# Kernel tuning notes

Measured on AMD Instinct MI355X. Metric: run time of the kernel, lower is better.

The kernel has to match this reference:

```python
import jax, jax.numpy as jnp
import numpy as np

WINDOW = (7, 7)
SHIFT = (3, 3)
NUM_HEADS = 4
DIM = 128


def _rel_pos_index():
    wh, ww = WINDOW
    coords = np.stack(np.meshgrid(np.arange(wh), np.arange(ww), indexing='ij'))  # [2,wh,ww]
    cf = coords.reshape(2, -1)                    # [2, N]
    rc = (cf[:, :, None] - cf[:, None, :]).transpose(1, 2, 0)  # [N,N,2]
    rc[:, :, 0] += wh - 1
    rc[:, :, 1] += ww - 1
    rc[:, :, 0] *= 2 * ww - 1
    return jnp.asarray(rc.sum(-1).reshape(-1))    # [N*N] int


def _attn_mask_np(pH, pW, sh):
    # Static-shape shift mask (host-side numpy; constant under jit).
    wh, ww = WINDOW
    m = np.zeros((pH, pW))
    h_slices = ((0, pH - wh), (pH - wh, pH - sh[0]), (pH - sh[0], pH))
    w_slices = ((0, pW - ww), (pW - ww, pW - sh[1]), (pW - sh[1], pW))
    cnt = 0
    for hs in h_slices:
        for ws in w_slices:
            m[hs[0]:hs[1], ws[0]:ws[1]] = cnt
            cnt += 1
    m = m.reshape(pH // wh, wh, pW // ww, ww).transpose(0, 2, 1, 3).reshape(-1, wh * ww)
    diff = m[:, None, :] - m[:, :, None]          # [num_windows, N, N]
    return jnp.asarray(np.where(diff != 0, -100.0, 0.0), dtype=np.float32)


def setup_inputs() -> dict:
    key = jax.random.key(0)
    ks = jax.random.split(key, 9)
    B, H, W, C = 32, 56, 56, DIM
    return {
        'input_q': jax.random.normal(ks[0], (B, H, W, C), jnp.float32),
        'input_k': jax.random.normal(ks[1], (B, H, W, C), jnp.float32),
        'input_v': jax.random.normal(ks[2], (B, H, W, C), jnp.float32),
        'q_weight': jax.random.normal(ks[3], (C, C), jnp.float32) * 0.05,
        'q_bias': jnp.zeros((C,), jnp.float32),
        'k_weight': jax.random.normal(ks[4], (C, C), jnp.float32) * 0.05,
        'k_bias': jnp.zeros((C,), jnp.float32),
        'v_weight': jax.random.normal(ks[5], (C, C), jnp.float32) * 0.05,
        'v_bias': jnp.zeros((C,), jnp.float32),
        'proj_weight': jax.random.normal(ks[6], (C, C), jnp.float32) * 0.05,
        'proj_bias': jnp.zeros((C,), jnp.float32),
        'rpb_table': jax.random.normal(ks[7], ((2 * WINDOW[0] - 1) * (2 * WINDOW[1] - 1), NUM_HEADS), jnp.float32) * 0.02,
    }


def reference(input_q, input_k, input_v, q_weight, q_bias, k_weight, k_bias,
              v_weight, v_bias, proj_weight, proj_bias, rpb_table):
    B, H, W, C = input_q.shape
    wh, ww = WINDOW
    pad_b = (wh - H % wh) % wh
    pad_r = (ww - W % ww) % ww
    pad = lambda t: jnp.pad(t, ((0, 0), (0, pad_b), (0, pad_r), (0, 0)))
    qx, kx, vx = pad(input_q), pad(input_k), pad(input_v)
    pad_H, pad_W = H + pad_b, W + pad_r
    sh = [0 if wh >= pad_H else SHIFT[0], 0 if ww >= pad_W else SHIFT[1]]
    if sum(sh) > 0:
        roll = lambda t: jnp.roll(t, (-sh[0], -sh[1]), axis=(1, 2))
        qx, kx, vx = roll(qx), roll(kx), roll(vx)
    nWh, nWw = pad_H // wh, pad_W // ww
    num_windows = nWh * nWw
    N = wh * ww

    def part(t):  # [B,pH,pW,C] -> [B*num_windows, N, C]
        t = t.reshape(B, nWh, wh, nWw, ww, C).transpose(0, 1, 3, 2, 4, 5)
        return t.reshape(B * num_windows, N, C)

    qx, kx, vx = part(qx), part(kx), part(vx)
    hd = C // NUM_HEADS

    def heads(x, w, b):  # linear + split heads -> [BW, nH, N, hd]
        return (x @ w.T + b).reshape(-1, N, NUM_HEADS, hd).transpose(0, 2, 1, 3)

    q = heads(qx, q_weight, q_bias) * (hd ** -0.5)
    k = heads(kx, k_weight, k_bias)
    v = heads(vx, v_weight, v_bias)

    attn = jnp.einsum('whqd,whkd->whqk', q, k)    # [BW, nH, N, N]
    rpb = rpb_table[_rel_pos_index()].reshape(N, N, NUM_HEADS).transpose(2, 0, 1)[None]
    attn = attn + rpb
    if sum(sh) > 0:
        mask = _attn_mask_np(pad_H, pad_W, sh)    # [num_windows, N, N]
        attn = attn.reshape(B, num_windows, NUM_HEADS, N, N) + mask[None, :, None]
        attn = attn.reshape(B * num_windows, NUM_HEADS, N, N)
    attn = jax.nn.softmax(attn, axis=-1)

    x = jnp.einsum('whqk,whkd->whqd', attn, v).transpose(0, 2, 1, 3).reshape(B * num_windows, N, C)
    x = x @ proj_weight.T + proj_bias
    x = x.reshape(B, nWh, nWw, wh, ww, C).transpose(0, 1, 3, 2, 4, 5).reshape(B, pad_H, pad_W, C)
    if sum(sh) > 0:
        x = jnp.roll(x, (sh[0], sh[1]), axis=(1, 2))
    return x[:, :H, :W, :]
```

## Files before the change

### kernel.cpp

```cpp
#include <hip/hip_runtime.h>
#include <hip/hip_bf16.h>

typedef __attribute__((ext_vector_type(8))) short s16x8;
typedef __attribute__((ext_vector_type(4))) float f32x4;
typedef __attribute__((ext_vector_type(16))) float f32x16;
typedef __attribute__((ext_vector_type(2))) unsigned int u32x2;
typedef __attribute__((ext_vector_type(4))) unsigned int u32x4;

#define MFMA16(a, b, c) __builtin_amdgcn_mfma_f32_16x16x32_bf16((a), (b), (c), 0, 0, 0)
#define MFMA32(a, b, c) __builtin_amdgcn_mfma_f32_32x32x16_bf16((a), (b), (c), 0, 0, 0)
#define LOG2E 1.4426950408889634f

static __device__ __forceinline__ unsigned int pk2(float a, float b) {
  union { __hip_bfloat162 h2; unsigned int u; } cv;
  cv.h2 = __float22bfloat162_rn(make_float2(a, b));
  return cv.u;
}
static __device__ __forceinline__ int div7(int x) { return (x * 9363) >> 16; }
static __device__ __forceinline__ int swz256(int row, int byteoff) {
  return row * 256 + (byteoff ^ ((row & 7) << 4));
}
static __device__ __forceinline__ int swz128(int row, int byteoff) {
  return row * 128 + (byteoff ^ ((row & 7) << 4));
}

__global__ void swin_prep(const float* __restrict__ wq, const float* __restrict__ wk,
                          const float* __restrict__ wv, const float* __restrict__ wp,
                          const float* __restrict__ rpb_table,
                          unsigned short* __restrict__ wsW, float* __restrict__ rpbm) {
  int idx = blockIdx.x * 256 + threadIdx.x;
  if (idx < 65536) {
    int t = idx >> 14, loc = idx & 16383;
    const float* s = (t == 0) ? wq : (t == 1) ? wk : (t == 2) ? wv : wp;
    union { __hip_bfloat16 h; unsigned short u; } cv;
    cv.h = __float2bfloat16(s[loc]);
    wsW[idx] = cv.u;
  } else {
    int k = idx - 65536;
    int c = k >> 14;
    int h = (k >> 12) & 3;
    int i = (k >> 6) & 63, j = k & 63;
    float val;
    if (j >= 49) val = -1e30f;
    else if (i >= 49) val = 0.f;
    else {
      int yi = div7(i), xi = i - yi * 7;
      int yj = div7(j), xj = j - yj * 7;
      int ridx = (yi - yj + 6) * 13 + (xi - xj + 6);
      val = rpb_table[ridx * 4 + h];
      int cwi = c >> 1, cwj = c & 1;
      int rgi = (cwi ? (yi < 4 ? 3 : 6) : 0) + (cwj ? (xi < 4 ? 1 : 2) : 0);
      int rgj = (cwi ? (yj < 4 ? 3 : 6) : 0) + (cwj ? (xj < 4 ? 1 : 2) : 0);
      if (rgi != rgj) val -= 100.f;
      val *= LOG2E;
    }
    rpbm[k] = val;
  }
}

__global__ __launch_bounds__(512, 6) void swin_main(
    const float* __restrict__ xq, const float* __restrict__ xk, const float* __restrict__ xv,
    const float* __restrict__ bq, const float* __restrict__ bk, const float* __restrict__ bv,
    const float* __restrict__ bp, const unsigned short* __restrict__ wsW,
    const float* __restrict__ rpbm, float* __restrict__ out) {
  __shared__ __align__(16) char sm[49152];

  const int tid = threadIdx.x;
  const int lane = tid & 63;
  const int wv_ = tid >> 6;
  const int l15 = lane & 15;
  const int lg = lane >> 4;
  const int kgrp = lg * 8;
  const int rsub = lg * 4;
  const int l31 = lane & 31;
  const int hi = lane >> 5;

  const int bid = blockIdx.x;
  const int b = bid >> 6;
  const int widx = bid & 63;
  const int wi = widx >> 3, wj = widx & 7;
  const long obase = (long)b * 56 * 56 * 128;
  const int mcase = ((wi == 7) ? 2 : 0) + ((wj == 7) ? 1 : 0);

  const int xrow = tid >> 3;
  const int xk16 = (tid & 7) << 4;
  long xoff = -1;
  if (xrow < 49) {
    int ty = div7(xrow), tx = xrow - ty * 7;
    int ih = wi * 7 + ty + 3; if (ih >= 56) ih -= 56;
    int iw = wj * 7 + tx + 3; if (iw >= 56) iw -= 56;
    xoff = obase + (long)((ih * 56 + iw) * 128 + xk16);
  }
  {
    float ra[16], rb[16], rc[16];
#pragma unroll
    for (int i = 0; i < 16; ++i) { ra[i] = 0.f; rb[i] = 0.f; rc[i] = 0.f; }
    if (xoff >= 0) {
#pragma unroll
      for (int q = 0; q < 4; ++q) {
        f32x4 v = *(const f32x4*)(xq + xoff + q * 4);
        ra[q*4+0]=v[0]; ra[q*4+1]=v[1]; ra[q*4+2]=v[2]; ra[q*4+3]=v[3];
      }
#pragma unroll
      for (int q = 0; q < 4; ++q) {
        f32x4 v = *(const f32x4*)(xk + xoff + q * 4);
        rb[q*4+0]=v[0]; rb[q*4+1]=v[1]; rb[q*4+2]=v[2]; rb[q*4+3]=v[3];
      }
#pragma unroll
      for (int q = 0; q < 4; ++q) {
        f32x4 v = *(const f32x4*)(xv + xoff + q * 4);
        rc[q*4+0]=v[0]; rc[q*4+1]=v[1]; rc[q*4+2]=v[2]; rc[q*4+3]=v[3];
      }
    }
    auto wrx = [&](int base, float* r) {
      unsigned int w[8];
#pragma unroll
      for (int i = 0; i < 8; ++i) w[i] = pk2(r[2*i], r[2*i+1]);
      u32x4 a = {w[0], w[1], w[2], w[3]};
      u32x4 bb = {w[4], w[5], w[6], w[7]};
      *(u32x4*)(sm + base + swz256(xrow, xk16 * 2)) = a;
      *(u32x4*)(sm + base + swz256(xrow, xk16 * 2 + 16)) = bb;
    };
    wrx(0, ra);
    wrx(16384, rb);
    wrx(32768, rc);
  }
  __syncthreads();

  const float QSCALE = 0.17677669529663687f * LOG2E;
  unsigned int qpk[4][2], kpk[4][2], vpk[4][2];
  {
    const int nrow = wv_ * 16 + l15;
    {
      s16x8 afr[4];
#pragma unroll
      for (int kt = 0; kt < 4; ++kt)
        afr[kt] = *(const s16x8*)(wsW + nrow * 128 + kt * 32 + kgrp);
      f32x4 bv4 = *(const f32x4*)(bq + wv_ * 16 + rsub);
#pragma unroll
      for (int tt = 0; tt < 4; ++tt) {
        f32x4 acc = {0.f, 0.f, 0.f, 0.f};
#pragma unroll
        for (int kt = 0; kt < 4; ++kt) {
          s16x8 bfr = *(const s16x8*)(sm + swz256(tt * 16 + l15, (kt * 32 + kgrp) * 2));
          acc = MFMA16(afr[kt], bfr, acc);
        }
        qpk[tt][0] = pk2(acc[0] * QSCALE + bv4[0] * QSCALE, acc[1] * QSCALE + bv4[1] * QSCALE);
        qpk[tt][1] = pk2(acc[2] * QSCALE + bv4[2] * QSCALE, acc[3] * QSCALE + bv4[3] * QSCALE);
      }
    }
    {
      s16x8 afr[4];
#pragma unroll
      for (int kt = 0; kt < 4; ++kt)
        afr[kt] = *(const s16x8*)(wsW + 16384 + nrow * 128 + kt * 32 + kgrp);
      f32x4 bv4 = *(const f32x4*)(bk + wv_ * 16 + rsub);
#pragma unroll
      for (int tt = 0; tt < 4; ++tt) {
        f32x4 acc = {0.f, 0.f, 0.f, 0.f};
#pragma unroll
        for (int kt = 0; kt < 4; ++kt) {
          s16x8 bfr = *(const s16x8*)(sm + 16384 + swz256(tt * 16 + l15, (kt * 32 + kgrp) * 2));
          acc = MFMA16(afr[kt], bfr, acc);
        }
        kpk[tt][0] = pk2(acc[0] + bv4[0], acc[1] + bv4[1]);
        kpk[tt][1] = pk2(acc[2] + bv4[2], acc[3] + bv4[3]);
      }
    }
    {
      s16x8 bfrw[4];
#pragma unroll
      for (int kt = 0; kt < 4; ++kt)
        bfrw[kt] = *(const s16x8*)(wsW + 32768 + nrow * 128 + kt * 32 + kgrp);
      float bval = bv[nrow];
#pragma unroll
      for (int mt = 0; mt < 4; ++mt) {
        f32x4 acc = {0.f, 0.f, 0.f, 0.f};
#pragma unroll
        for (int kt = 0; kt < 4; ++kt) {
          s16x8 afr = *(const s16x8*)(sm + 32768 + swz256(mt * 16 + l15, (kt * 32 + kgrp) * 2));
          acc = MFMA16(afr, bfrw[kt], acc);
        }
        vpk[mt][0] = pk2(acc[0] + bval, acc[1] + bval);
        vpk[mt][1] = pk2(acc[2] + bval, acc[3] + bval);
      }
    }
  }
  __syncthreads();

#pragma unroll
  for (int tt = 0; tt < 4; ++tt) {
    u32x2 w = {qpk[tt][0], qpk[tt][1]};
    *(u32x2*)(sm + swz256(tt * 16 + l15, 2 * (wv_ * 16 + rsub))) = w;
  }
#pragma unroll
  for (int tt = 0; tt < 4; ++tt) {
    u32x2 w = {kpk[tt][0], kpk[tt][1]};
    *(u32x2*)(sm + 16384 + swz256(tt * 16 + l15, 2 * (wv_ * 16 + rsub))) = w;
  }
#pragma unroll
  for (int mt = 0; mt < 4; ++mt) {
    u32x2 w = {vpk[mt][0], vpk[mt][1]};
    *(u32x2*)(sm + 32768 + swz128(wv_ * 16 + l15, 2 * (mt * 16 + rsub))) = w;
  }
  __syncthreads();

  const int h = wv_ & 3;
  const int half = wv_ >> 2;
  const int coff = h * 32;
  unsigned int pu[2][4][2];
  f32x16 O;
  {
    const float* rpbm_h = rpbm + (((mcase << 2) + h) << 12) + (half * 32 + l31) * 64 + 4 * hi;
    f32x16 S[2];
#pragma unroll
    for (int t = 0; t < 2; ++t)
#pragma unroll
      for (int g = 0; g < 4; ++g) {
        f32x4 rv = *(const f32x4*)(rpbm_h + t * 32 + g * 8);
        S[t][g*4+0] = rv[0]; S[t][g*4+1] = rv[1];
        S[t][g*4+2] = rv[2]; S[t][g*4+3] = rv[3];
      }
    s16x8 qfr[2], kfr[2][2];
#pragma unroll
    for (int s = 0; s < 2; ++s) {
      qfr[s] = *(const s16x8*)(sm + swz256(half * 32 + l31, 2 * (coff + s * 16 + hi * 8)));
#pragma unroll
      for (int t = 0; t < 2; ++t)
        kfr[t][s] = *(const s16x8*)(sm + 16384 + swz256(t * 32 + l31, 2 * (coff + s * 16 + hi * 8)));
    }
#pragma unroll
    for (int s = 0; s < 2; ++s) {
      S[0] = MFMA32(kfr[0][s], qfr[s], S[0]);
      S[1] = MFMA32(kfr[1][s], qfr[s], S[1]);
    }
    float m = S[0][0];
#pragma unroll
    for (int t = 0; t < 2; ++t)
#pragma unroll
      for (int r = 0; r < 16; ++r) m = fmaxf(m, S[t][r]);
    m = fmaxf(m, __shfl_xor(m, 32));
    float sum = 0.f;
#pragma unroll
    for (int t = 0; t < 2; ++t)
#pragma unroll
      for (int r = 0; r < 16; ++r) { float e = exp2f(S[t][r] - m); S[t][r] = e; sum += e; }
    sum += __shfl_xor(sum, 32);
    float inv = 1.0f / sum;
#pragma unroll
    for (int t = 0; t < 2; ++t)
#pragma unroll
      for (int g = 0; g < 4; ++g) {
        pu[t][g][0] = pk2(S[t][g*4+0] * inv, S[t][g*4+1] * inv);
        pu[t][g][1] = pk2(S[t][g*4+2] * inv, S[t][g*4+3] * inv);
      }
    O = (f32x16)0.f;
#pragma unroll
    for (int s = 0; s < 4; ++s) {
      const int t = s >> 1, gb = (s & 1) * 2;
      unsigned int own0 = pu[t][gb + hi][0], own1 = pu[t][gb + hi][1];
      unsigned int po0 = __shfl_xor(pu[t][gb + 1 - hi][0], 32);
      unsigned int po1 = __shfl_xor(pu[t][gb + 1 - hi][1], 32);
      union { u32x4 u; s16x8 s; } pf;
      pf.u = hi ? (u32x4){po0, po1, own0, own1} : (u32x4){own0, own1, po0, po1};
      s16x8 vfr = *(const s16x8*)(sm + 32768 + swz128(coff + l31, 2 * (s * 16 + hi * 8)));
      O = MFMA32(vfr, pf.s, O);
    }
  }
  __syncthreads();

#pragma unroll
  for (int g = 0; g < 4; ++g) {
    u32x2 w = {pk2(O[g*4+0], O[g*4+1]), pk2(O[g*4+2], O[g*4+3])};
    *(u32x2*)(sm + swz256(half * 32 + l31, 2 * (coff + g * 8 + 4 * hi))) = w;
  }
  __syncthreads();

  {
    const int nrow = wv_ * 16 + l15;
    s16x8 afr[4];
#pragma unroll
    for (int kt = 0; kt < 4; ++kt)
      afr[kt] = *(const s16x8*)(wsW + 49152 + nrow * 128 + kt * 32 + kgrp);
    f32x4 bv4 = *(const f32x4*)(bp + wv_ * 16 + rsub);
#pragma unroll
    for (int tt = 0; tt < 4; ++tt) {
      f32x4 acc = {0.f, 0.f, 0.f, 0.f};
#pragma unroll
      for (int kt = 0; kt < 4; ++kt) {
        s16x8 bfr = *(const s16x8*)(sm + swz256(tt * 16 + l15, (kt * 32 + kgrp) * 2));
        acc = MFMA16(afr[kt], bfr, acc);
      }
      int tok = tt * 16 + l15;
      if (tok < 49) {
        int ty = div7(tok), tx = tok - ty * 7;
        int oh = wi * 7 + ty + 3; if (oh >= 56) oh -= 56;
        int ow = wj * 7 + tx + 3; if (ow >= 56) ow -= 56;
        f32x4 res = {acc[0] + bv4[0], acc[1] + bv4[1], acc[2] + bv4[2], acc[3] + bv4[3]};
        *(f32x4*)(out + obase + (oh * 56 + ow) * 128 + wv_ * 16 + rsub) = res;
      }
    }
  }
}

extern "C" void kernel_launch(void* const* d_in, const int* in_sizes, int n_in,
                              void* d_out, int out_size, void* d_ws, size_t ws_size,
                              hipStream_t stream) {
  const float* xq = (const float*)d_in[0];
  const float* xk = (const float*)d_in[1];
  const float* xv = (const float*)d_in[2];
  const float* wq = (const float*)d_in[3];
  const float* bq = (const float*)d_in[4];
  const float* wk = (const float*)d_in[5];
  const float* bk = (const float*)d_in[6];
  const float* wv = (const float*)d_in[7];
  const float* bv = (const float*)d_in[8];
  const float* wp = (const float*)d_in[9];
  const float* bp = (const float*)d_in[10];
  const float* rpb = (const float*)d_in[11];

  unsigned short* wsW = (unsigned short*)d_ws;
  float* rpbm = (float*)((char*)d_ws + 131072);

  swin_prep<<<512, 256, 0, stream>>>(wq, wk, wv, wp, rpb, wsW, rpbm);

  float* out = (float*)d_out;
  swin_main<<<2048, 512, 0, stream>>>(xq, xk, xv, bq, bk, bv, bp, wsW, rpbm, out);
}
```

Measured before the change: 82.90 us.

## Process two windows per block with prefetched inputs for the second window

Each block now handles two consecutive windows instead of one, halving the grid. The global loads of the second window's q/k/v inputs are issued before the first window's attention so their latency overlaps compute, and a separate LDS region for the attention output lets the second window's inputs be staged while the first is projected. The cost is more LDS per block (64KB vs 48KB), fewer resident blocks per CU (launch bound lowered to 4), and higher register pressure from the prefetch buffers.

```diff
diff --git a/kernel.cpp b/kernel.cpp
--- a/kernel.cpp
+++ b/kernel.cpp
@@ -58,12 +58,12 @@
   }
 }
 
-__global__ __launch_bounds__(512, 6) void swin_main(
+__global__ __launch_bounds__(512, 4) void swin_main(
     const float* __restrict__ xq, const float* __restrict__ xk, const float* __restrict__ xv,
     const float* __restrict__ bq, const float* __restrict__ bk, const float* __restrict__ bv,
     const float* __restrict__ bp, const unsigned short* __restrict__ wsW,
     const float* __restrict__ rpbm, float* __restrict__ out) {
-  __shared__ __align__(16) char sm[49152];
+  __shared__ __align__(16) char sm[65536];
 
   const int tid = threadIdx.x;
   const int lane = tid & 63;
@@ -76,60 +76,51 @@
   const int hi = lane >> 5;
 
   const int bid = blockIdx.x;
-  const int b = bid >> 6;
-  const int widx = bid & 63;
-  const int wi = widx >> 3, wj = widx & 7;
+  const int b = bid >> 5;
+  const int w0 = (bid & 31) << 1;
   const long obase = (long)b * 56 * 56 * 128;
-  const int mcase = ((wi == 7) ? 2 : 0) + ((wj == 7) ? 1 : 0);
 
   const int xrow = tid >> 3;
   const int xk16 = (tid & 7) << 4;
-  long xoff = -1;
-  if (xrow < 49) {
+
+  auto xoff_of = [&](int w) -> long {
+    if (xrow >= 49) return -1;
+    int wi = w >> 3, wj = w & 7;
     int ty = div7(xrow), tx = xrow - ty * 7;
     int ih = wi * 7 + ty + 3; if (ih >= 56) ih -= 56;
     int iw = wj * 7 + tx + 3; if (iw >= 56) iw -= 56;
-    xoff = obase + (long)((ih * 56 + iw) * 128 + xk16);
-  }
-  {
-    float ra[16], rb[16], rc[16];
-#pragma unroll
-    for (int i = 0; i < 16; ++i) { ra[i] = 0.f; rb[i] = 0.f; rc[i] = 0.f; }
-    if (xoff >= 0) {
+    return obase + (long)((ih * 56 + iw) * 128 + xk16);
+  };
+  const long xoffA = xoff_of(w0);
+  const long xoffB = xoff_of(w0 + 1);
+
+  float px[16], py[16], pz[16];
+
+  auto load16 = [&](const float* src, long off, float* r) {
+#pragma unroll
+    for (int i = 0; i < 16; ++i) r[i] = 0.f;
+    if (off >= 0) {
 #pragma unroll
       for (int q = 0; q < 4; ++q) {
-        f32x4 v = *(const f32x4*)(xq + xoff + q * 4);
-        ra[q*4+0]=v[0]; ra[q*4+1]=v[1]; ra[q*4+2]=v[2]; ra[q*4+3]=v[3];
-      }
-#pragma unroll
-      for (int q = 0; q < 4; ++q) {
-        f32x4 v = *(const f32x4*)(xk + xoff + q * 4);
-        rb[q*4+0]=v[0]; rb[q*4+1]=v[1]; rb[q*4+2]=v[2]; rb[q*4+3]=v[3];
-      }
-#pragma unroll
-      for (int q = 0; q < 4; ++q) {
-        f32x4 v = *(const f32x4*)(xv + xoff + q * 4);
-        rc[q*4+0]=v[0]; rc[q*4+1]=v[1]; rc[q*4+2]=v[2]; rc[q*4+3]=v[3];
-      }
-    }
-    auto wrx = [&](int base, float* r) {
-      unsigned int w[8];
-#pragma unroll
-      for (int i = 0; i < 8; ++i) w[i] = pk2(r[2*i], r[2*i+1]);
-      u32x4 a = {w[0], w[1], w[2], w[3]};
-      u32x4 bb = {w[4], w[5], w[6], w[7]};
-      *(u32x4*)(sm + base + swz256(xrow, xk16 * 2)) = a;
-      *(u32x4*)(sm + base + swz256(xrow, xk16 * 2 + 16)) = bb;
-    };
-    wrx(0, ra);
-    wrx(16384, rb);
-    wrx(32768, rc);
-  }
-  __syncthreads();
+        f32x4 v = *(const f32x4*)(src + off + q * 4);
+        r[q*4+0]=v[0]; r[q*4+1]=v[1]; r[q*4+2]=v[2]; r[q*4+3]=v[3];
+      }
+    }
+  };
+  auto wrx = [&](int base, const float* r) {
+    unsigned int w[8];
+#pragma unroll
+    for (int i = 0; i < 8; ++i) w[i] = pk2(r[2*i], r[2*i+1]);
+    u32x4 a = {w[0], w[1], w[2], w[3]};
+    u32x4 bb2 = {w[4], w[5], w[6], w[7]};
+    *(u32x4*)(sm + base + swz256(xrow, xk16 * 2)) = a;
+    *(u32x4*)(sm + base + swz256(xrow, xk16 * 2 + 16)) = bb2;
+  };
 
   const float QSCALE = 0.17677669529663687f * LOG2E;
   unsigned int qpk[4][2], kpk[4][2], vpk[4][2];
-  {
+
+  auto proj_qkv = [&]() {
     const int nrow = wv_ * 16 + l15;
     {
       s16x8 afr[4];
@@ -185,32 +176,32 @@
         vpk[mt][1] = pk2(acc[2] + bval, acc[3] + bval);
       }
     }
-  }
-  __syncthreads();
-
-#pragma unroll
-  for (int tt = 0; tt < 4; ++tt) {
-    u32x2 w = {qpk[tt][0], qpk[tt][1]};
-    *(u32x2*)(sm + swz256(tt * 16 + l15, 2 * (wv_ * 16 + rsub))) = w;
-  }
-#pragma unroll
-  for (int tt = 0; tt < 4; ++tt) {
-    u32x2 w = {kpk[tt][0], kpk[tt][1]};
-    *(u32x2*)(sm + 16384 + swz256(tt * 16 + l15, 2 * (wv_ * 16 + rsub))) = w;
-  }
-#pragma unroll
-  for (int mt = 0; mt < 4; ++mt) {
-    u32x2 w = {vpk[mt][0], vpk[mt][1]};
-    *(u32x2*)(sm + 32768 + swz128(wv_ * 16 + l15, 2 * (mt * 16 + rsub))) = w;
-  }
-  __syncthreads();
+  };
+
+  auto write_qkv = [&]() {
+#pragma unroll
+    for (int tt = 0; tt < 4; ++tt) {
+      u32x2 w = {qpk[tt][0], qpk[tt][1]};
+      *(u32x2*)(sm + swz256(tt * 16 + l15, 2 * (wv_ * 16 + rsub))) = w;
+    }
+#pragma unroll
+    for (int tt = 0; tt < 4; ++tt) {
+      u32x2 w = {kpk[tt][0], kpk[tt][1]};
+      *(u32x2*)(sm + 16384 + swz256(tt * 16 + l15, 2 * (wv_ * 16 + rsub))) = w;
+    }
+#pragma unroll
+    for (int mt = 0; mt < 4; ++mt) {
+      u32x2 w = {vpk[mt][0], vpk[mt][1]};
+      *(u32x2*)(sm + 32768 + swz128(wv_ * 16 + l15, 2 * (mt * 16 + rsub))) = w;
+    }
+  };
 
   const int h = wv_ & 3;
   const int half = wv_ >> 2;
   const int coff = h * 32;
-  unsigned int pu[2][4][2];
-  f32x16 O;
-  {
+
+  auto attention = [&](int w, f32x16& O) {
+    const int mcase = (((w >> 3) == 7) ? 2 : 0) + (((w & 7) == 7) ? 1 : 0);
     const float* rpbm_h = rpbm + (((mcase << 2) + h) << 12) + (half * 32 + l31) * 64 + 4 * hi;
     f32x16 S[2];
 #pragma unroll
@@ -247,6 +238,7 @@
       for (int r = 0; r < 16; ++r) { float e = exp2f(S[t][r] - m); S[t][r] = e; sum += e; }
     sum += __shfl_xor(sum, 32);
     float inv = 1.0f / sum;
+    unsigned int pu[2][4][2];
 #pragma unroll
     for (int t = 0; t < 2; ++t)
 #pragma unroll
@@ -266,17 +258,18 @@
       s16x8 vfr = *(const s16x8*)(sm + 32768 + swz128(coff + l31, 2 * (s * 16 + hi * 8)));
       O = MFMA32(vfr, pf.s, O);
     }
-  }
-  __syncthreads();
-
-#pragma unroll
-  for (int g = 0; g < 4; ++g) {
-    u32x2 w = {pk2(O[g*4+0], O[g*4+1]), pk2(O[g*4+2], O[g*4+3])};
-    *(u32x2*)(sm + swz256(half * 32 + l31, 2 * (coff + g * 8 + 4 * hi))) = w;
-  }
-  __syncthreads();
-
-  {
+  };
+
+  auto writeO = [&](const f32x16& O) {
+#pragma unroll
+    for (int g = 0; g < 4; ++g) {
+      u32x2 w = {pk2(O[g*4+0], O[g*4+1]), pk2(O[g*4+2], O[g*4+3])};
+      *(u32x2*)(sm + 49152 + swz256(half * 32 + l31, 2 * (coff + g * 8 + 4 * hi))) = w;
+    }
+  };
+
+  auto proj_scatter = [&](int w) {
+    const int wi = w >> 3, wj = w & 7;
     const int nrow = wv_ * 16 + l15;
     s16x8 afr[4];
 #pragma unroll
@@ -288,7 +281,7 @@
       f32x4 acc = {0.f, 0.f, 0.f, 0.f};
 #pragma unroll
       for (int kt = 0; kt < 4; ++kt) {
-        s16x8 bfr = *(const s16x8*)(sm + swz256(tt * 16 + l15, (kt * 32 + kgrp) * 2));
+        s16x8 bfr = *(const s16x8*)(sm + 49152 + swz256(tt * 16 + l15, (kt * 32 + kgrp) * 2));
         acc = MFMA16(afr[kt], bfr, acc);
       }
       int tok = tt * 16 + l15;
@@ -300,7 +293,33 @@
         *(f32x4*)(out + obase + (oh * 56 + ow) * 128 + wv_ * 16 + rsub) = res;
       }
     }
-  }
+  };
+
+  f32x16 Oacc;
+
+  load16(xq, xoffA, px); load16(xk, xoffA, py); load16(xv, xoffA, pz);
+  wrx(0, px); wrx(16384, py); wrx(32768, pz);
+  __syncthreads();
+  proj_qkv();
+  __syncthreads();
+  write_qkv();
+  __syncthreads();
+  load16(xq, xoffB, px); load16(xk, xoffB, py); load16(xv, xoffB, pz);
+  attention(w0, Oacc);
+  __syncthreads();
+  writeO(Oacc);
+  wrx(0, px); wrx(16384, py); wrx(32768, pz);
+  __syncthreads();
+  proj_scatter(w0);
+  proj_qkv();
+  __syncthreads();
+  write_qkv();
+  __syncthreads();
+  attention(w0 + 1, Oacc);
+  __syncthreads();
+  writeO(Oacc);
+  __syncthreads();
+  proj_scatter(w0 + 1);
 }
 
 extern "C" void kernel_launch(void* const* d_in, const int* in_sizes, int n_in,
@@ -325,5 +344,5 @@
   swin_prep<<<512, 256, 0, stream>>>(wq, wk, wv, wp, rpb, wsW, rpbm);
 
   float* out = (float*)d_out;
-  swin_main<<<2048, 512, 0, stream>>>(xq, xk, xv, bq, bk, bv, bp, wsW, rpbm, out);
-}
+  swin_main<<<1024, 512, 0, stream>>>(xq, xk, xv, bq, bk, bv, bp, wsW, rpbm, out);
+}
```

After: 103.8 us. 1.25x slower.

## Split fused Swin kernel into QKV projection and attention kernels via workspace

Applied to the files above, without the earlier changes.

Splits the single fused kernel into two: one computes the Q/K/V projections and writes a pre-swizzled bf16 LDS image per window to workspace, and the second loads that image straight into LDS with global_load_lds and runs attention plus the output projection. The aim is to shorten each kernel and lower register pressure so occupancy and overlap improve. In exchange it adds about 100 MB of extra global write and read traffic and a second launch. The old fused kernel stays as a fallback when the workspace is too small.

```diff
diff --git a/kernel.cpp b/kernel.cpp
--- a/kernel.cpp
+++ b/kernel.cpp
@@ -22,6 +22,11 @@
 }
 static __device__ __forceinline__ int swz128(int row, int byteoff) {
   return row * 128 + (byteoff ^ ((row & 7) << 4));
+}
+static __device__ __forceinline__ void gload16(const void* g, void* l) {
+  __builtin_amdgcn_global_load_lds(
+      (const __attribute__((address_space(1))) unsigned int*)g,
+      (__attribute__((address_space(3))) unsigned int*)l, 16, 0, 0);
 }
 
 __global__ void swin_prep(const float* __restrict__ wq, const float* __restrict__ wk,
@@ -58,11 +63,134 @@
   }
 }
 
-__global__ __launch_bounds__(512, 6) void swin_main(
+__global__ __launch_bounds__(512, 6) void swin_qkv(
     const float* __restrict__ xq, const float* __restrict__ xk, const float* __restrict__ xv,
     const float* __restrict__ bq, const float* __restrict__ bk, const float* __restrict__ bv,
-    const float* __restrict__ bp, const unsigned short* __restrict__ wsW,
-    const float* __restrict__ rpbm, float* __restrict__ out) {
+    const unsigned short* __restrict__ wsW, char* __restrict__ qkvimg) {
+  __shared__ __align__(16) char sm[49152];
+
+  const int tid = threadIdx.x;
+  const int lane = tid & 63;
+  const int wv_ = tid >> 6;
+  const int l15 = lane & 15;
+  const int lg = lane >> 4;
+  const int kgrp = lg * 8;
+  const int rsub = lg * 4;
+
+  const int bid = blockIdx.x;
+  const int b = bid >> 6;
+  const int widx = bid & 63;
+  const int wi = widx >> 3, wj = widx & 7;
+  const long obase = (long)b * 56 * 56 * 128;
+
+  const int xrow = tid >> 3;
+  const int xk16 = (tid & 7) << 4;
+  long xoff = -1;
+  if (xrow < 49) {
+    int ty = div7(xrow), tx = xrow - ty * 7;
+    int ih = wi * 7 + ty + 3; if (ih >= 56) ih -= 56;
+    int iw = wj * 7 + tx + 3; if (iw >= 56) iw -= 56;
+    xoff = obase + (long)((ih * 56 + iw) * 128 + xk16);
+  }
+  {
+    float ra[16], rb[16], rc[16];
+#pragma unroll
+    for (int i = 0; i < 16; ++i) { ra[i] = 0.f; rb[i] = 0.f; rc[i] = 0.f; }
+    if (xoff >= 0) {
+#pragma unroll
+      for (int q = 0; q < 4; ++q) {
+        f32x4 v = *(const f32x4*)(xq + xoff + q * 4);
+        ra[q*4+0]=v[0]; ra[q*4+1]=v[1]; ra[q*4+2]=v[2]; ra[q*4+3]=v[3];
+      }
+#pragma unroll
+      for (int q = 0; q < 4; ++q) {
+        f32x4 v = *(const f32x4*)(xk + xoff + q * 4);
+        rb[q*4+0]=v[0]; rb[q*4+1]=v[1]; rb[q*4+2]=v[2]; rb[q*4+3]=v[3];
+      }
+#pragma unroll
+      for (int q = 0; q < 4; ++q) {
+        f32x4 v = *(const f32x4*)(xv + xoff + q * 4);
+        rc[q*4+0]=v[0]; rc[q*4+1]=v[1]; rc[q*4+2]=v[2]; rc[q*4+3]=v[3];
+      }
+    }
+    auto wrx = [&](int base, const float* r) {
+      unsigned int w[8];
+#pragma unroll
+      for (int i = 0; i < 8; ++i) w[i] = pk2(r[2*i], r[2*i+1]);
+      u32x4 a = {w[0], w[1], w[2], w[3]};
+      u32x4 bb2 = {w[4], w[5], w[6], w[7]};
+      *(u32x4*)(sm + base + swz256(xrow, xk16 * 2)) = a;
+      *(u32x4*)(sm + base + swz256(xrow, xk16 * 2 + 16)) = bb2;
+    };
+    wrx(0, ra); wrx(16384, rb); wrx(32768, rc);
+  }
+  __syncthreads();
+
+  const float QSCALE = 0.17677669529663687f * LOG2E;
+  const long wb = (long)bid * 49152;
+  const int nrow = wv_ * 16 + l15;
+  {
+    s16x8 afr[4];
+#pragma unroll
+    for (int kt = 0; kt < 4; ++kt)
+      afr[kt] = *(const s16x8*)(wsW + nrow * 128 + kt * 32 + kgrp);
+    f32x4 bv4 = *(const f32x4*)(bq + wv_ * 16 + rsub);
+#pragma unroll
+    for (int tt = 0; tt < 4; ++tt) {
+      f32x4 acc = {0.f, 0.f, 0.f, 0.f};
+#pragma unroll
+      for (int kt = 0; kt < 4; ++kt) {
+        s16x8 bfr = *(const s16x8*)(sm + swz256(tt * 16 + l15, (kt * 32 + kgrp) * 2));
+        acc = MFMA16(afr[kt], bfr, acc);
+      }
+      u32x2 w = {pk2((acc[0] + bv4[0]) * QSCALE, (acc[1] + bv4[1]) * QSCALE),
+                 pk2((acc[2] + bv4[2]) * QSCALE, (acc[3] + bv4[3]) * QSCALE)};
+      *(u32x2*)(qkvimg + wb + swz256(tt * 16 + l15, 2 * (wv_ * 16 + rsub))) = w;
+    }
+  }
+  {
+    s16x8 afr[4];
+#pragma unroll
+    for (int kt = 0; kt < 4; ++kt)
+      afr[kt] = *(const s16x8*)(wsW + 16384 + nrow * 128 + kt * 32 + kgrp);
+    f32x4 bv4 = *(const f32x4*)(bk + wv_ * 16 + rsub);
+#pragma unroll
+    for (int tt = 0; tt < 4; ++tt) {
+      f32x4 acc = {0.f, 0.f, 0.f, 0.f};
+#pragma unroll
+      for (int kt = 0; kt < 4; ++kt) {
+        s16x8 bfr = *(const s16x8*)(sm + 16384 + swz256(tt * 16 + l15, (kt * 32 + kgrp) * 2));
+        acc = MFMA16(afr[kt], bfr, acc);
+      }
+      u32x2 w = {pk2(acc[0] + bv4[0], acc[1] + bv4[1]),
+                 pk2(acc[2] + bv4[2], acc[3] + bv4[3])};
+      *(u32x2*)(qkvimg + wb + 16384 + swz256(tt * 16 + l15, 2 * (wv_ * 16 + rsub))) = w;
+    }
+  }
+  {
+    s16x8 bfrw[4];
+#pragma unroll
+    for (int kt = 0; kt < 4; ++kt)
+      bfrw[kt] = *(const s16x8*)(wsW + 32768 + nrow * 128 + kt * 32 + kgrp);
+    float bval = bv[nrow];
+#pragma unroll
+    for (int mt = 0; mt < 4; ++mt) {
+      f32x4 acc = {0.f, 0.f, 0.f, 0.f};
+#pragma unroll
+      for (int kt = 0; kt < 4; ++kt) {
+        s16x8 afr = *(const s16x8*)(sm + 32768 + swz256(mt * 16 + l15, (kt * 32 + kgrp) * 2));
+        acc = MFMA16(afr, bfrw[kt], acc);
+      }
+      u32x2 w = {pk2(acc[0] + bval, acc[1] + bval), pk2(acc[2] + bval, acc[3] + bval)};
+      *(u32x2*)(qkvimg + wb + 32768 + swz128(nrow, 2 * (mt * 16 + rsub))) = w;
+    }
+  }
+}
+
+__global__ __launch_bounds__(512, 6) void swin_attn(
+    const char* __restrict__ qkvimg, const float* __restrict__ bp,
+    const unsigned short* __restrict__ wsW, const float* __restrict__ rpbm,
+    float* __restrict__ out) {
   __shared__ __align__(16) char sm[49152];
 
   const int tid = threadIdx.x;
@@ -82,6 +210,138 @@
   const long obase = (long)b * 56 * 56 * 128;
   const int mcase = ((wi == 7) ? 2 : 0) + ((wj == 7) ? 1 : 0);
 
+  {
+    const char* src = qkvimg + (long)bid * 49152 + wv_ * 6144 + lane * 16;
+#pragma unroll
+    for (int i = 0; i < 6; ++i)
+      gload16(src + i * 1024, sm + wv_ * 6144 + i * 1024);
+  }
+
+  const int h = wv_ & 3;
+  const int half = wv_ >> 2;
+  const int coff = h * 32;
+
+  const float* rpbm_h = rpbm + (((mcase << 2) + h) << 12) + (half * 32 + l31) * 64 + 4 * hi;
+  f32x16 S[2];
+#pragma unroll
+  for (int t = 0; t < 2; ++t)
+#pragma unroll
+    for (int g = 0; g < 4; ++g) {
+      f32x4 rv = *(const f32x4*)(rpbm_h + t * 32 + g * 8);
+      S[t][g*4+0] = rv[0]; S[t][g*4+1] = rv[1];
+      S[t][g*4+2] = rv[2]; S[t][g*4+3] = rv[3];
+    }
+  __syncthreads();
+
+  f32x16 O;
+  {
+    s16x8 qfr[2], kfr[2][2];
+#pragma unroll
+    for (int s = 0; s < 2; ++s) {
+      qfr[s] = *(const s16x8*)(sm + swz256(half * 32 + l31, 2 * (coff + s * 16 + hi * 8)));
+#pragma unroll
+      for (int t = 0; t < 2; ++t)
+        kfr[t][s] = *(const s16x8*)(sm + 16384 + swz256(t * 32 + l31, 2 * (coff + s * 16 + hi * 8)));
+    }
+#pragma unroll
+    for (int s = 0; s < 2; ++s) {
+      S[0] = MFMA32(kfr[0][s], qfr[s], S[0]);
+      S[1] = MFMA32(kfr[1][s], qfr[s], S[1]);
+    }
+    float m = S[0][0];
+#pragma unroll
+    for (int t = 0; t < 2; ++t)
+#pragma unroll
+      for (int r = 0; r < 16; ++r) m = fmaxf(m, S[t][r]);
+    m = fmaxf(m, __shfl_xor(m, 32));
+    float sum = 0.f;
+#pragma unroll
+    for (int t = 0; t < 2; ++t)
+#pragma unroll
+      for (int r = 0; r < 16; ++r) { float e = exp2f(S[t][r] - m); S[t][r] = e; sum += e; }
+    sum += __shfl_xor(sum, 32);
+    float inv = 1.0f / sum;
+    unsigned int pu[2][4][2];
+#pragma unroll
+    for (int t = 0; t < 2; ++t)
+#pragma unroll
+      for (int g = 0; g < 4; ++g) {
+        pu[t][g][0] = pk2(S[t][g*4+0] * inv, S[t][g*4+1] * inv);
+        pu[t][g][1] = pk2(S[t][g*4+2] * inv, S[t][g*4+3] * inv);
+      }
+    O = (f32x16)0.f;
+#pragma unroll
+    for (int s = 0; s < 4; ++s) {
+      const int t = s >> 1, gb = (s & 1) * 2;
+      unsigned int own0 = pu[t][gb + hi][0], own1 = pu[t][gb + hi][1];
+      unsigned int po0 = __shfl_xor(pu[t][gb + 1 - hi][0], 32);
+      unsigned int po1 = __shfl_xor(pu[t][gb + 1 - hi][1], 32);
+      union { u32x4 u; s16x8 s; } pf;
+      pf.u = hi ? (u32x4){po0, po1, own0, own1} : (u32x4){own0, own1, po0, po1};
+      s16x8 vfr = *(const s16x8*)(sm + 32768 + swz128(coff + l31, 2 * (s * 16 + hi * 8)));
+      O = MFMA32(vfr, pf.s, O);
+    }
+  }
+  __syncthreads();
+
+#pragma unroll
+  for (int g = 0; g < 4; ++g) {
+    u32x2 w = {pk2(O[g*4+0], O[g*4+1]), pk2(O[g*4+2], O[g*4+3])};
+    *(u32x2*)(sm + swz256(half * 32 + l31, 2 * (coff + g * 8 + 4 * hi))) = w;
+  }
+  __syncthreads();
+
+  {
+    const int nrow = wv_ * 16 + l15;
+    s16x8 afr[4];
+#pragma unroll
+    for (int kt = 0; kt < 4; ++kt)
+      afr[kt] = *(const s16x8*)(wsW + 49152 + nrow * 128 + kt * 32 + kgrp);
+    f32x4 bv4 = *(const f32x4*)(bp + wv_ * 16 + rsub);
+#pragma unroll
+    for (int tt = 0; tt < 4; ++tt) {
+      f32x4 acc = {0.f, 0.f, 0.f, 0.f};
+#pragma unroll
+      for (int kt = 0; kt < 4; ++kt) {
+        s16x8 bfr = *(const s16x8*)(sm + swz256(tt * 16 + l15, (kt * 32 + kgrp) * 2));
+        acc = MFMA16(afr[kt], bfr, acc);
+      }
+      int tok = tt * 16 + l15;
+      if (tok < 49) {
+        int ty = div7(tok), tx = tok - ty * 7;
+        int oh = wi * 7 + ty + 3; if (oh >= 56) oh -= 56;
+        int ow = wj * 7 + tx + 3; if (ow >= 56) ow -= 56;
+        f32x4 res = {acc[0] + bv4[0], acc[1] + bv4[1], acc[2] + bv4[2], acc[3] + bv4[3]};
+        *(f32x4*)(out + obase + (oh * 56 + ow) * 128 + wv_ * 16 + rsub) = res;
+      }
+    }
+  }
+}
+
+__global__ __launch_bounds__(512, 6) void swin_main(
+    const float* __restrict__ xq, const float* __restrict__ xk, const float* __restrict__ xv,
+    const float* __restrict__ bq, const float* __restrict__ bk, const float* __restrict__ bv,
+    const float* __restrict__ bp, const unsigned short* __restrict__ wsW,
+    const float* __restrict__ rpbm, float* __restrict__ out) {
+  __shared__ __align__(16) char sm[49152];
+
+  const int tid = threadIdx.x;
+  const int lane = tid & 63;
+  const int wv_ = tid >> 6;
+  const int l15 = lane & 15;
+  const int lg = lane >> 4;
+  const int kgrp = lg * 8;
+  const int rsub = lg * 4;
+  const int l31 = lane & 31;
+  const int hi = lane >> 5;
+
+  const int bid = blockIdx.x;
+  const int b = bid >> 6;
+  const int widx = bid & 63;
+  const int wi = widx >> 3, wj = widx & 7;
+  const long obase = (long)b * 56 * 56 * 128;
+  const int mcase = ((wi == 7) ? 2 : 0) + ((wj == 7) ? 1 : 0);
+
   const int xrow = tid >> 3;
   const int xk16 = (tid & 7) << 4;
   long xoff = -1;
@@ -112,18 +372,16 @@
         rc[q*4+0]=v[0]; rc[q*4+1]=v[1]; rc[q*4+2]=v[2]; rc[q*4+3]=v[3];
       }
     }
-    auto wrx = [&](int base, float* r) {
+    auto wrx = [&](int base, const float* r) {
       unsigned int w[8];
 #pragma unroll
       for (int i = 0; i < 8; ++i) w[i] = pk2(r[2*i], r[2*i+1]);
       u32x4 a = {w[0], w[1], w[2], w[3]};
-      u32x4 bb = {w[4], w[5], w[6], w[7]};
+      u32x4 bb2 = {w[4], w[5], w[6], w[7]};
       *(u32x4*)(sm + base + swz256(xrow, xk16 * 2)) = a;
-      *(u32x4*)(sm + base + swz256(xrow, xk16 * 2 + 16)) = bb;
+      *(u32x4*)(sm + base + swz256(xrow, xk16 * 2 + 16)) = bb2;
     };
-    wrx(0, ra);
-    wrx(16384, rb);
-    wrx(32768, rc);
+    wrx(0, ra); wrx(16384, rb); wrx(32768, rc);
   }
   __syncthreads();
 
@@ -145,8 +403,8 @@
           s16x8 bfr = *(const s16x8*)(sm + swz256(tt * 16 + l15, (kt * 32 + kgrp) * 2));
           acc = MFMA16(afr[kt], bfr, acc);
         }
-        qpk[tt][0] = pk2(acc[0] * QSCALE + bv4[0] * QSCALE, acc[1] * QSCALE + bv4[1] * QSCALE);
-        qpk[tt][1] = pk2(acc[2] * QSCALE + bv4[2] * QSCALE, acc[3] * QSCALE + bv4[3] * QSCALE);
+        qpk[tt][0] = pk2((acc[0] + bv4[0]) * QSCALE, (acc[1] + bv4[1]) * QSCALE);
+        qpk[tt][1] = pk2((acc[2] + bv4[2]) * QSCALE, (acc[3] + bv4[3]) * QSCALE);
       }
     }
     {
@@ -208,7 +466,6 @@
   const int h = wv_ & 3;
   const int half = wv_ >> 2;
   const int coff = h * 32;
-  unsigned int pu[2][4][2];
   f32x16 O;
   {
     const float* rpbm_h = rpbm + (((mcase << 2) + h) << 12) + (half * 32 + l31) * 64 + 4 * hi;
@@ -247,6 +504,7 @@
       for (int r = 0; r < 16; ++r) { float e = exp2f(S[t][r] - m); S[t][r] = e; sum += e; }
     sum += __shfl_xor(sum, 32);
     float inv = 1.0f / sum;
+    unsigned int pu[2][4][2];
 #pragma unroll
     for (int t = 0; t < 2; ++t)
 #pragma unroll
@@ -321,9 +579,16 @@
 
   unsigned short* wsW = (unsigned short*)d_ws;
   float* rpbm = (float*)((char*)d_ws + 131072);
+  char* qkvimg = (char*)d_ws + 393216;
+  const size_t NEED = 393216ull + 2048ull * 49152ull;
 
   swin_prep<<<512, 256, 0, stream>>>(wq, wk, wv, wp, rpb, wsW, rpbm);
 
   float* out = (float*)d_out;
-  swin_main<<<2048, 512, 0, stream>>>(xq, xk, xv, bq, bk, bv, bp, wsW, rpbm, out);
-}
+  if (ws_size >= NEED) {
+    swin_qkv<<<2048, 512, 0, stream>>>(xq, xk, xv, bq, bk, bv, wsW, qkvimg);
+    swin_attn<<<2048, 512, 0, stream>>>(qkvimg, bp, wsW, rpbm, out);
+  } else {
+    swin_main<<<2048, 512, 0, stream>>>(xq, xk, xv, bq, bk, bv, bp, wsW, rpbm, out);
+  }
+}
```

Measured after the change: 132.4 us. +59.7%, slower.

## Stage input loads via global_load_lds DMA overlapped with projection GEMMs

Applied to the files above, without the earlier changes.

Replaces the register-staged fp32 loads of the q/k/v windows with direct global-to-LDS DMA (global_load_lds). Each input is then converted to bf16 in LDS, and the DMA of the next input is issued while the current projection GEMM runs, so global latency overlaps with MFMA work. V staging and the O write are moved to reorder the barriers. This adds several __syncthreads and an extra LDS round trip per input, and now uses a 32 KB fp32 staging region.

```diff
diff --git a/kernel.cpp b/kernel.cpp
--- a/kernel.cpp
+++ b/kernel.cpp
@@ -22,6 +22,11 @@
 }
 static __device__ __forceinline__ int swz128(int row, int byteoff) {
   return row * 128 + (byteoff ^ ((row & 7) << 4));
+}
+static __device__ __forceinline__ void gload16(const void* g, void* l) {
+  __builtin_amdgcn_global_load_lds(
+      (const __attribute__((address_space(1))) unsigned int*)g,
+      (__attribute__((address_space(3))) unsigned int*)l, 16, 0, 0);
 }
 
 __global__ void swin_prep(const float* __restrict__ wq, const float* __restrict__ wk,
@@ -82,112 +87,102 @@
   const long obase = (long)b * 56 * 56 * 128;
   const int mcase = ((wi == 7) ? 2 : 0) + ((wj == 7) ? 1 : 0);
 
-  const int xrow = tid >> 3;
-  const int xk16 = (tid & 7) << 4;
-  long xoff = -1;
-  if (xrow < 49) {
-    int ty = div7(xrow), tx = xrow - ty * 7;
-    int ih = wi * 7 + ty + 3; if (ih >= 56) ih -= 56;
-    int iw = wj * 7 + tx + 3; if (iw >= 56) iw -= 56;
-    xoff = obase + (long)((ih * 56 + iw) * 128 + xk16);
-  }
-  {
-    float ra[16], rb[16], rc[16];
-#pragma unroll
-    for (int i = 0; i < 16; ++i) { ra[i] = 0.f; rb[i] = 0.f; rc[i] = 0.f; }
-    if (xoff >= 0) {
-#pragma unroll
-      for (int q = 0; q < 4; ++q) {
-        f32x4 v = *(const f32x4*)(xq + xoff + q * 4);
-        ra[q*4+0]=v[0]; ra[q*4+1]=v[1]; ra[q*4+2]=v[2]; ra[q*4+3]=v[3];
-      }
-#pragma unroll
-      for (int q = 0; q < 4; ++q) {
-        f32x4 v = *(const f32x4*)(xk + xoff + q * 4);
-        rb[q*4+0]=v[0]; rb[q*4+1]=v[1]; rb[q*4+2]=v[2]; rb[q*4+3]=v[3];
-      }
-#pragma unroll
-      for (int q = 0; q < 4; ++q) {
-        f32x4 v = *(const f32x4*)(xv + xoff + q * 4);
-        rc[q*4+0]=v[0]; rc[q*4+1]=v[1]; rc[q*4+2]=v[2]; rc[q*4+3]=v[3];
-      }
-    }
-    auto wrx = [&](int base, float* r) {
-      unsigned int w[8];
-#pragma unroll
-      for (int i = 0; i < 8; ++i) w[i] = pk2(r[2*i], r[2*i+1]);
-      u32x4 a = {w[0], w[1], w[2], w[3]};
-      u32x4 bb = {w[4], w[5], w[6], w[7]};
-      *(u32x4*)(sm + base + swz256(xrow, xk16 * 2)) = a;
-      *(u32x4*)(sm + base + swz256(xrow, xk16 * 2 + 16)) = bb;
-    };
-    wrx(0, ra);
-    wrx(16384, rb);
-    wrx(32768, rc);
-  }
-  __syncthreads();
+  long dsrc[4];
+#pragma unroll
+  for (int i = 0; i < 4; ++i) {
+    int tok = wv_ * 8 + i * 2 + hi;
+    long off = 0;
+    if (tok < 49) {
+      int ty = div7(tok), tx = tok - ty * 7;
+      int ih = wi * 7 + ty + 3; if (ih >= 56) ih -= 56;
+      int iw = wj * 7 + tx + 3; if (iw >= 56) iw -= 56;
+      off = (long)(ih * 56 + iw) * 512;
+    }
+    dsrc[i] = obase * 4 + off + (long)l31 * 16;
+  }
+  auto dma_x = [&](const float* src) {
+    const char* s8 = (const char*)src;
+#pragma unroll
+    for (int i = 0; i < 4; ++i)
+      gload16(s8 + dsrc[i], sm + wv_ * 4096 + i * 1024);
+  };
+
+  const int ctok = tid >> 3;
+  const int cch16 = (tid & 7) << 4;
+  auto cvt_x = [&]() {
+    u32x4 a, bb;
+    if (ctok < 49) {
+      const char* fp = sm + ctok * 512 + (tid & 7) * 64;
+      f32x4 v0 = *(const f32x4*)(fp);
+      f32x4 v1 = *(const f32x4*)(fp + 16);
+      f32x4 v2 = *(const f32x4*)(fp + 32);
+      f32x4 v3 = *(const f32x4*)(fp + 48);
+      a = (u32x4){pk2(v0[0], v0[1]), pk2(v0[2], v0[3]), pk2(v1[0], v1[1]), pk2(v1[2], v1[3])};
+      bb = (u32x4){pk2(v2[0], v2[1]), pk2(v2[2], v2[3]), pk2(v3[0], v3[1]), pk2(v3[2], v3[3])};
+    } else {
+      a = (u32x4){0, 0, 0, 0};
+      bb = (u32x4){0, 0, 0, 0};
+    }
+    *(u32x4*)(sm + 32768 + swz256(ctok, cch16 * 2)) = a;
+    *(u32x4*)(sm + 32768 + swz256(ctok, cch16 * 2 + 16)) = bb;
+  };
 
   const float QSCALE = 0.17677669529663687f * LOG2E;
+  const int nrow = wv_ * 16 + l15;
+
   unsigned int qpk[4][2], kpk[4][2], vpk[4][2];
-  {
-    const int nrow = wv_ * 16 + l15;
-    {
-      s16x8 afr[4];
-#pragma unroll
-      for (int kt = 0; kt < 4; ++kt)
-        afr[kt] = *(const s16x8*)(wsW + nrow * 128 + kt * 32 + kgrp);
-      f32x4 bv4 = *(const f32x4*)(bq + wv_ * 16 + rsub);
-#pragma unroll
-      for (int tt = 0; tt < 4; ++tt) {
-        f32x4 acc = {0.f, 0.f, 0.f, 0.f};
-#pragma unroll
-        for (int kt = 0; kt < 4; ++kt) {
-          s16x8 bfr = *(const s16x8*)(sm + swz256(tt * 16 + l15, (kt * 32 + kgrp) * 2));
-          acc = MFMA16(afr[kt], bfr, acc);
-        }
-        qpk[tt][0] = pk2(acc[0] * QSCALE + bv4[0] * QSCALE, acc[1] * QSCALE + bv4[1] * QSCALE);
-        qpk[tt][1] = pk2(acc[2] * QSCALE + bv4[2] * QSCALE, acc[3] * QSCALE + bv4[3] * QSCALE);
-      }
-    }
-    {
-      s16x8 afr[4];
-#pragma unroll
-      for (int kt = 0; kt < 4; ++kt)
-        afr[kt] = *(const s16x8*)(wsW + 16384 + nrow * 128 + kt * 32 + kgrp);
-      f32x4 bv4 = *(const f32x4*)(bk + wv_ * 16 + rsub);
-#pragma unroll
-      for (int tt = 0; tt < 4; ++tt) {
-        f32x4 acc = {0.f, 0.f, 0.f, 0.f};
-#pragma unroll
-        for (int kt = 0; kt < 4; ++kt) {
-          s16x8 bfr = *(const s16x8*)(sm + 16384 + swz256(tt * 16 + l15, (kt * 32 + kgrp) * 2));
-          acc = MFMA16(afr[kt], bfr, acc);
-        }
-        kpk[tt][0] = pk2(acc[0] + bv4[0], acc[1] + bv4[1]);
-        kpk[tt][1] = pk2(acc[2] + bv4[2], acc[3] + bv4[3]);
-      }
-    }
-    {
-      s16x8 bfrw[4];
-#pragma unroll
-      for (int kt = 0; kt < 4; ++kt)
-        bfrw[kt] = *(const s16x8*)(wsW + 32768 + nrow * 128 + kt * 32 + kgrp);
-      float bval = bv[nrow];
-#pragma unroll
-      for (int mt = 0; mt < 4; ++mt) {
-        f32x4 acc = {0.f, 0.f, 0.f, 0.f};
-#pragma unroll
-        for (int kt = 0; kt < 4; ++kt) {
-          s16x8 afr = *(const s16x8*)(sm + 32768 + swz256(mt * 16 + l15, (kt * 32 + kgrp) * 2));
-          acc = MFMA16(afr, bfrw[kt], acc);
-        }
-        vpk[mt][0] = pk2(acc[0] + bval, acc[1] + bval);
-        vpk[mt][1] = pk2(acc[2] + bval, acc[3] + bval);
-      }
-    }
-  }
-  __syncthreads();
-
+  auto gemmT = [&](int woff, const float* bias, float scale, unsigned int dst[4][2]) {
+    s16x8 afr[4];
+#pragma unroll
+    for (int kt = 0; kt < 4; ++kt)
+      afr[kt] = *(const s16x8*)(wsW + woff + nrow * 128 + kt * 32 + kgrp);
+    f32x4 bv4 = *(const f32x4*)(bias + wv_ * 16 + rsub);
+#pragma unroll
+    for (int tt = 0; tt < 4; ++tt) {
+      f32x4 acc = {0.f, 0.f, 0.f, 0.f};
+#pragma unroll
+      for (int kt = 0; kt < 4; ++kt) {
+        s16x8 bfr = *(const s16x8*)(sm + 32768 + swz256(tt * 16 + l15, (kt * 32 + kgrp) * 2));
+        acc = MFMA16(afr[kt], bfr, acc);
+      }
+      dst[tt][0] = pk2((acc[0] + bv4[0]) * scale, (acc[1] + bv4[1]) * scale);
+      dst[tt][1] = pk2((acc[2] + bv4[2]) * scale, (acc[3] + bv4[3]) * scale);
+    }
+  };
+  auto gemmV = [&](int woff, const float* bias) {
+    s16x8 bfrw[4];
+#pragma unroll
+    for (int kt = 0; kt < 4; ++kt)
+      bfrw[kt] = *(const s16x8*)(wsW + woff + nrow * 128 + kt * 32 + kgrp);
+    float bval = bias[nrow];
+#pragma unroll
+    for (int mt = 0; mt < 4; ++mt) {
+      f32x4 acc = {0.f, 0.f, 0.f, 0.f};
+#pragma unroll
+      for (int kt = 0; kt < 4; ++kt) {
+        s16x8 afr = *(const s16x8*)(sm + 32768 + swz256(mt * 16 + l15, (kt * 32 + kgrp) * 2));
+        acc = MFMA16(afr, bfrw[kt], acc);
+      }
+      vpk[mt][0] = pk2(acc[0] + bval, acc[1] + bval);
+      vpk[mt][1] = pk2(acc[2] + bval, acc[3] + bval);
+    }
+  };
+
+  dma_x(xq);
+  __syncthreads();
+  cvt_x();
+  __syncthreads();
+  dma_x(xk);
+  gemmT(0, bq, QSCALE, qpk);
+  __syncthreads();
+  cvt_x();
+  __syncthreads();
+  dma_x(xv);
+  gemmT(16384, bk, 1.f, kpk);
+  __syncthreads();
+  cvt_x();
+  __syncthreads();
+  gemmV(32768, bv);
 #pragma unroll
   for (int tt = 0; tt < 4; ++tt) {
     u32x2 w = {qpk[tt][0], qpk[tt][1]};
@@ -197,11 +192,6 @@
   for (int tt = 0; tt < 4; ++tt) {
     u32x2 w = {kpk[tt][0], kpk[tt][1]};
     *(u32x2*)(sm + 16384 + swz256(tt * 16 + l15, 2 * (wv_ * 16 + rsub))) = w;
-  }
-#pragma unroll
-  for (int mt = 0; mt < 4; ++mt) {
-    u32x2 w = {vpk[mt][0], vpk[mt][1]};
-    *(u32x2*)(sm + 32768 + swz128(wv_ * 16 + l15, 2 * (mt * 16 + rsub))) = w;
   }
   __syncthreads();
 
@@ -209,8 +199,12 @@
   const int half = wv_ >> 2;
   const int coff = h * 32;
   unsigned int pu[2][4][2];
-  f32x16 O;
   {
+#pragma unroll
+    for (int mt = 0; mt < 4; ++mt) {
+      u32x2 w = {vpk[mt][0], vpk[mt][1]};
+      *(u32x2*)(sm + 32768 + swz128(wv_ * 16 + l15, 2 * (mt * 16 + rsub))) = w;
+    }
     const float* rpbm_h = rpbm + (((mcase << 2) + h) << 12) + (half * 32 + l31) * 64 + 4 * hi;
     f32x16 S[2];
 #pragma unroll
@@ -254,7 +248,11 @@
         pu[t][g][0] = pk2(S[t][g*4+0] * inv, S[t][g*4+1] * inv);
         pu[t][g][1] = pk2(S[t][g*4+2] * inv, S[t][g*4+3] * inv);
       }
-    O = (f32x16)0.f;
+  }
+  __syncthreads();
+
+  {
+    f32x16 O = (f32x16)0.f;
 #pragma unroll
     for (int s = 0; s < 4; ++s) {
       const int t = s >> 1, gb = (s & 1) * 2;
@@ -266,18 +264,15 @@
       s16x8 vfr = *(const s16x8*)(sm + 32768 + swz128(coff + l31, 2 * (s * 16 + hi * 8)));
       O = MFMA32(vfr, pf.s, O);
     }
-  }
-  __syncthreads();
-
-#pragma unroll
-  for (int g = 0; g < 4; ++g) {
-    u32x2 w = {pk2(O[g*4+0], O[g*4+1]), pk2(O[g*4+2], O[g*4+3])};
-    *(u32x2*)(sm + swz256(half * 32 + l31, 2 * (coff + g * 8 + 4 * hi))) = w;
+#pragma unroll
+    for (int g = 0; g < 4; ++g) {
+      u32x2 w = {pk2(O[g*4+0], O[g*4+1]), pk2(O[g*4+2], O[g*4+3])};
+      *(u32x2*)(sm + swz256(half * 32 + l31, 2 * (coff + g * 8 + 4 * hi))) = w;
+    }
   }
   __syncthreads();
 
   {
-    const int nrow = wv_ * 16 + l15;
     s16x8 afr[4];
 #pragma unroll
     for (int kt = 0; kt < 4; ++kt)
```

Result: slower. 89.78 us (+8.3%).
